# Kernel tuning notes

Measured on AMD Instinct MI355X. Metric: run time of the kernel, lower is better.

The kernel has to match this reference:

```python
import jax, jax.numpy as jnp
import numpy as np

B, F, H, C, K, NHID = 4096, 512, 1024, 100, 32, 3  # NHID = num_layers - 1 hidden->hidden layers


def setup_inputs() -> dict:
    key = jax.random.key(0)
    ks = jax.random.split(key, 5)
    s_in = 1.0 / np.sqrt(F)
    s_h = 1.0 / np.sqrt(H)
    return {
        "x": jax.random.normal(ks[0], (B, F), dtype=jnp.float32),
        "W_in": jax.random.normal(ks[1], (K, F, H), dtype=jnp.float32) * s_in,
        "b_in": jnp.zeros((K, H), dtype=jnp.float32),
        "W_hid": jax.random.normal(ks[2], (NHID, K, H, H), dtype=jnp.float32) * s_h,
        "b_hid": jnp.zeros((NHID, K, H), dtype=jnp.float32),
        "W_out": jax.random.normal(ks[3], (K, H, C), dtype=jnp.float32) * s_h,
        "b_out": jnp.zeros((K, C), dtype=jnp.float32),
    }


def reference(x, W_in, b_in, W_hid, b_hid, W_out, b_out):
    # Batched ensemble: all k MLPs as stacked GEMMs. Dropout off (inference).
    h = jax.nn.relu(jnp.einsum("bf,kfh->kbh", x, W_in) + b_in[:, None, :])  # [K,B,H]
    for i in range(W_hid.shape[0]):  # small fixed layer loop
        h = jax.nn.relu(jnp.einsum("kbh,khj->kbj", h, W_hid[i]) + b_hid[i][:, None, :])
    logits = jnp.einsum("kbh,khc->kbc", h, W_out) + b_out[:, None, :]  # [K,B,C]
    return jnp.mean(logits, axis=0)  # [B,C]
```

## Files before the change

kernel.cpp:

```cpp
#include <hip/hip_runtime.h>
#include <stdint.h>

#define BB   4096
#define FF   512
#define HH   1024
#define CC   100
#define KE   32
#define NHIDL 3
#define CPAD 128

typedef __attribute__((ext_vector_type(8))) short short8;
typedef __attribute__((ext_vector_type(4))) float float4_t;

__device__ __forceinline__ unsigned short f2h(float f) {
  _Float16 h = (_Float16)f;
  union { _Float16 h; unsigned short u; } cv;
  cv.h = h;
  return cv.u;
}

__device__ __forceinline__ void gll16(const void* g, void* l) {
  __builtin_amdgcn_global_load_lds((const __attribute__((address_space(1))) void*)g,
                                   (__attribute__((address_space(3))) void*)l,
                                   16, 0, 0);
}

__global__ void cvt_f16(const float* __restrict__ in, unsigned short* __restrict__ out, int n4) {
  int i = blockIdx.x * 256 + threadIdx.x;
  if (i < n4) {
    float4 v = ((const float4*)in)[i];
    ushort4 o;
    o.x = f2h(v.x); o.y = f2h(v.y); o.z = f2h(v.z); o.w = f2h(v.w);
    ((ushort4*)out)[i] = o;
  }
}

__global__ void transpose_cvt(const float* __restrict__ in, unsigned short* __restrict__ out,
                              int R, int C, int Cpad) {
  __shared__ float tile[32][33];
  int b = blockIdx.z;
  const float* ib = in + (size_t)b * R * C;
  unsigned short* ob = out + (size_t)b * Cpad * R;
  int c0 = blockIdx.x * 32, r0 = blockIdx.y * 32;
  int tx = threadIdx.x & 31, ty = threadIdx.x >> 5;
#pragma unroll
  for (int j = 0; j < 4; ++j) {
    int r = r0 + ty + j * 8, c = c0 + tx;
    tile[ty + j * 8][tx] = (c < C) ? ib[(size_t)r * C + c] : 0.0f;
  }
  __syncthreads();
#pragma unroll
  for (int j = 0; j < 4; ++j) {
    int orow = c0 + ty + j * 8, ocol = r0 + tx;
    if (orow < Cpad) ob[(size_t)orow * R + ocol] = f2h(tile[tx][ty + j * 8]);
  }
}

__global__ void reduce_mean(const float* __restrict__ L, float* __restrict__ out,
                            int n, long long sk) {
  int i = blockIdx.x * 256 + threadIdx.x;
  if (i < n) {
    float s = 0.f;
#pragma unroll
    for (int k = 0; k < KE; ++k) s += L[(long long)k * sk + i];
    out[i] = s * (1.0f / (float)KE);
  }
}

template <int RELU, int FINAL, int KD>
__global__ __launch_bounds__(256, 4) void gemm_f16(
    const unsigned short* __restrict__ A, long long sAk,
    const unsigned short* __restrict__ Bt, long long sBk,
    const float* __restrict__ bias, int sBiasK,
    unsigned short* __restrict__ Out, long long sOutK,
    float* __restrict__ OutF, long long sFk) {
  const int t = threadIdx.x;
  const int lane = t & 63;
  const int wave = t >> 6;
  const int wm = wave & 1;
  const int wn = wave >> 1;
  const int kz = blockIdx.z;
  const int m0 = blockIdx.y * 128;
  const int n0 = blockIdx.x * 128;

  const unsigned short* Ab = A + (long long)kz * sAk + (long long)m0 * KD;
  const unsigned short* Bb = Bt + (long long)kz * sBk + (long long)n0 * KD;

  __shared__ __align__(16) unsigned short smA[128 * 64];
  __shared__ __align__(16) unsigned short smB[128 * 64];

  float4_t acc[4][4];
#pragma unroll
  for (int i = 0; i < 4; ++i)
#pragma unroll
    for (int j = 0; j < 4; ++j) acc[i][j] = (float4_t){0.f, 0.f, 0.f, 0.f};

  int goff[4];
  unsigned short* la[4];
  unsigned short* lb[4];
#pragma unroll
  for (int j = 0; j < 4; ++j) {
    int s = j * 256 + t;
    int row = s >> 3;
    int g = (s & 7) ^ (row & 7);
    goff[j] = row * KD + g * 8;
    la[j] = smA + (size_t)((j * 256 + (t & 0xC0)) * 8);
    lb[j] = smB + (size_t)((j * 256 + (t & 0xC0)) * 8);
  }

  const int r16 = lane & 15;
  const int q = lane >> 4;
  int offA[4][2], offB[4][2];
#pragma unroll
  for (int i = 0; i < 4; ++i) {
#pragma unroll
    for (int kh = 0; kh < 2; ++kh) {
      int ra = wm * 64 + i * 16 + r16;
      offA[i][kh] = ra * 64 + ((((kh * 4 + q)) ^ (ra & 7)) << 3);
      int rb = wn * 64 + i * 16 + r16;
      offB[i][kh] = rb * 64 + ((((kh * 4 + q)) ^ (rb & 7)) << 3);
    }
  }

#pragma unroll
  for (int kt = 0; kt < KD; kt += 64) {
#pragma unroll
    for (int j = 0; j < 4; ++j) gll16(Ab + goff[j] + kt, la[j]);
#pragma unroll
    for (int j = 0; j < 4; ++j) gll16(Bb + goff[j] + kt, lb[j]);
    __syncthreads();

#pragma unroll
    for (int kh = 0; kh < 2; ++kh) {
      short8 af[4], bf[4];
#pragma unroll
      for (int i = 0; i < 4; ++i) af[i] = *(const short8*)(smA + offA[i][kh]);
#pragma unroll
      for (int i = 0; i < 4; ++i) bf[i] = *(const short8*)(smB + offB[i][kh]);
#pragma unroll
      for (int mi = 0; mi < 4; ++mi)
#pragma unroll
        for (int ni = 0; ni < 4; ++ni)
          acc[mi][ni] = __builtin_amdgcn_mfma_f32_16x16x32_f16(af[mi], bf[ni], acc[mi][ni], 0, 0, 0);
    }
    __syncthreads();
  }

  const int rbase = q * 4;
  if (FINAL) {
#pragma unroll
    for (int ni = 0; ni < 4; ++ni) {
      int n = wn * 64 + ni * 16 + r16;
      if (n < CC) {
        float bv = bias[kz * sBiasK + n];
#pragma unroll
        for (int mi = 0; mi < 4; ++mi) {
#pragma unroll
          for (int r = 0; r < 4; ++r) {
            int m = m0 + wm * 64 + mi * 16 + rbase + r;
            OutF[(long long)kz * sFk + (long long)m * CC + n] = acc[mi][ni][r] + bv;
          }
        }
      }
    }
  } else {
#pragma unroll
    for (int ni = 0; ni < 4; ++ni) {
      int n = n0 + wn * 64 + ni * 16 + r16;
      float bv = bias[kz * sBiasK + n];
#pragma unroll
      for (int mi = 0; mi < 4; ++mi) {
        int m = m0 + wm * 64 + mi * 16 + rbase;
        unsigned short* op = Out + (long long)kz * sOutK + (long long)m * HH + n;
#pragma unroll
        for (int r = 0; r < 4; ++r) {
          float v = acc[mi][ni][r] + bv;
          if (RELU) v = fmaxf(v, 0.f);
          op[(long long)r * HH] = f2h(v);
        }
      }
    }
  }
}

template <int RELU, int KD>
__global__ __launch_bounds__(512, 2) void gemm256(
    const unsigned short* __restrict__ A, long long sAk,
    const unsigned short* __restrict__ Bt, long long sBk,
    const float* __restrict__ bias, int sBiasK,
    unsigned short* __restrict__ Out, long long sOutK) {
  static_assert(KD % 128 == 0, "need even K-tile count");
  const int t = threadIdx.x;
  const int lane = t & 63;
  const int wave = t >> 6;
  const int wm = wave >> 2;
  const int wn = wave & 3;
  const int r16 = lane & 15;
  const int q = lane >> 4;

  const int gx = gridDim.x, gy = gridDim.y;
  const int gxy = gx * gy;
  const int nwg = gxy * gridDim.z;
  int flat = blockIdx.x + gx * (blockIdx.y + gy * blockIdx.z);
  int id2 = (flat & 7) * (nwg >> 3) + (flat >> 3);
  const int kz = id2 / gxy;
  int rem = id2 - kz * gxy;
  const int ty = rem / gx;
  const int tx = rem - ty * gx;
  const int m0 = ty * 256;
  const int n0 = tx * 256;

  const unsigned short* Ab = A + (long long)kz * sAk + (long long)m0 * KD;
  const unsigned short* Bb = Bt + (long long)kz * sBk + (long long)n0 * KD;

  __shared__ __align__(16) unsigned short sm[2 * 32768];

  const int gq = (t >> 3) * KD + ((((t & 7) ^ ((t >> 3) & 7))) << 3);
  const int wbase = wave * 512;

  const int x7 = r16 & 7;
  const int xk0 = (q ^ x7) << 3;
  const int xk1 = ((4 + q) ^ x7) << 3;
  const int baseA = (wm * 128 + r16) * 64;
  const int baseB = (wn * 64 + r16) * 64;

  float4_t acc[8][4];
#pragma unroll
  for (int i = 0; i < 8; ++i)
#pragma unroll
    for (int j = 0; j < 4; ++j) acc[i][j] = (float4_t){0.f, 0.f, 0.f, 0.f};

  short8 af[4][2];
  short8 bf[4][2];

#define STGA(BUF, QI, TT) gll16(Ab + (QI) * 64 * KD + (TT) * 64 + gq, \
                                sm + (BUF) * 32768 + (QI) * 4096 + wbase)
#define STGB(BUF, QI, TT) gll16(Bb + (QI) * 64 * KD + (TT) * 64 + gq, \
                                sm + (BUF) * 32768 + 16384 + (QI) * 4096 + wbase)
#define DSA(BUF, MH) do { \
    const unsigned short* pA_ = sm + (BUF) * 32768 + baseA + (MH) * 4096; \
    _Pragma("unroll") for (int i_ = 0; i_ < 4; ++i_) { \
      af[i_][0] = *(const short8*)(pA_ + i_ * 1024 + xk0); \
      af[i_][1] = *(const short8*)(pA_ + i_ * 1024 + xk1); \
    } } while (0)
#define DSB(BUF, NH) do { \
    const unsigned short* pB_ = sm + (BUF) * 32768 + 16384 + baseB + (NH) * 2048; \
    _Pragma("unroll") for (int i_ = 0; i_ < 2; ++i_) { \
      bf[(NH) * 2 + i_][0] = *(const short8*)(pB_ + i_ * 1024 + xk0); \
      bf[(NH) * 2 + i_][1] = *(const short8*)(pB_ + i_ * 1024 + xk1); \
    } } while (0)
#define MM(MH, NH) do { \
    __builtin_amdgcn_s_setprio(1); \
    _Pragma("unroll") for (int kh_ = 0; kh_ < 2; ++kh_) { \
      _Pragma("unroll") for (int mi_ = 0; mi_ < 4; ++mi_) { \
        _Pragma("unroll") for (int ni_ = 0; ni_ < 2; ++ni_) { \
          acc[(MH) * 4 + mi_][(NH) * 2 + ni_] = __builtin_amdgcn_mfma_f32_16x16x32_f16( \
              af[mi_][kh_], bf[(NH) * 2 + ni_][kh_], acc[(MH) * 4 + mi_][(NH) * 2 + ni_], 0, 0, 0); \
        } } } \
    __builtin_amdgcn_s_setprio(0); } while (0)
#define BAR() asm volatile("s_barrier" ::: "memory")
#define VMCNT(n) asm volatile("s_waitcnt vmcnt(" #n ")" ::: "memory")

  STGA(0, 0, 0); STGA(0, 1, 0); STGA(0, 2, 0); STGA(0, 3, 0);
  STGB(0, 0, 0); STGB(0, 1, 0); STGB(0, 2, 0); STGB(0, 3, 0);
  STGA(1, 0, 1); STGA(1, 2, 1);
  STGB(1, 0, 1); STGB(1, 1, 1); STGB(1, 2, 1); STGB(1, 3, 1);
  VMCNT(6);
  BAR();

  const int nT = KD / 64;
  const int nI = nT / 2;
#pragma unroll 1
  for (int j = 0; j < nI - 1; ++j) {
    const int O1 = 2 * j + 1, E2 = 2 * j + 2, O2 = 2 * j + 3;
    DSA(0, 0); DSB(0, 0); STGA(1, 1, O1); STGA(1, 3, O1); MM(0, 0);           BAR();
    DSB(0, 1);            STGA(0, 0, E2); STGA(0, 2, E2); MM(0, 1);           BAR();
    DSA(0, 1);            STGB(0, 0, E2); STGB(0, 1, E2); MM(1, 1);           BAR();
                          STGB(0, 2, E2); STGB(0, 3, E2); MM(1, 0); VMCNT(6); BAR();
    DSA(1, 0); DSB(1, 0); STGA(0, 1, E2); STGA(0, 3, E2); MM(0, 0);           BAR();
    DSB(1, 1);            STGA(1, 0, O2); STGA(1, 2, O2); MM(0, 1);           BAR();
    DSA(1, 1);            STGB(1, 0, O2); STGB(1, 1, O2); MM(1, 1);           BAR();
                          STGB(1, 2, O2); STGB(1, 3, O2); MM(1, 0); VMCNT(6); BAR();
  }
  {
    const int O1 = nT - 1;
    DSA(0, 0); DSB(0, 0); STGA(1, 1, O1); STGA(1, 3, O1); MM(0, 0);           BAR();
    DSB(0, 1);                                            MM(0, 1);           BAR();
    DSA(0, 1);                                            MM(1, 1);           BAR();
                                                          MM(1, 0); VMCNT(0); BAR();
    DSA(1, 0); DSB(1, 0);                                 MM(0, 0);           BAR();
    DSB(1, 1);                                            MM(0, 1);           BAR();
    DSA(1, 1);                                            MM(1, 1);
                                                          MM(1, 0);
  }

  const int rbase = q * 4;
#pragma unroll
  for (int ni = 0; ni < 4; ++ni) {
    const int n = n0 + wn * 64 + ni * 16 + r16;
    const float bv = bias[kz * sBiasK + n];
#pragma unroll
    for (int mi = 0; mi < 8; ++mi) {
      const int m = m0 + wm * 128 + mi * 16 + rbase;
      unsigned short* op = Out + (long long)kz * sOutK + (long long)m * HH + n;
#pragma unroll
      for (int rr = 0; rr < 4; ++rr) {
        float v = acc[mi][ni][rr] + bv;
        if (RELU) v = fmaxf(v, 0.f);
        op[(long long)rr * HH] = f2h(v);
      }
    }
  }
#undef STGA
#undef STGB
#undef DSA
#undef DSB
#undef MM
#undef BAR
#undef VMCNT
}

extern "C" void kernel_launch(void* const* d_in, const int* in_sizes, int n_in,
                              void* d_out, int out_size, void* d_ws, size_t ws_size,
                              hipStream_t stream) {
  (void)in_sizes; (void)n_in; (void)out_size;
  const float* x     = (const float*)d_in[0];
  const float* W_in  = (const float*)d_in[1];
  const float* b_in  = (const float*)d_in[2];
  const float* W_hid = (const float*)d_in[3];
  const float* b_hid = (const float*)d_in[4];
  const float* W_out = (const float*)d_in[5];
  const float* b_out = (const float*)d_in[6];
  float* out = (float*)d_out;

  char* ws = (char*)d_ws;
  size_t off = 0;
  auto alloc = [&](size_t bytes) -> void* {
    void* p = ws + off;
    off += (bytes + 255) & ~(size_t)255;
    return p;
  };
  unsigned short* xb    = (unsigned short*)alloc((size_t)BB * FF * 2);
  unsigned short* WinT  = (unsigned short*)alloc((size_t)KE * HH * FF * 2);
  unsigned short* WhidT = (unsigned short*)alloc((size_t)NHIDL * KE * HH * HH * 2);
  unsigned short* WoutT = (unsigned short*)alloc((size_t)KE * CPAD * HH * 2);
  size_t fixed = off;

  int Bc = BB;
  while (Bc > 128 && fixed + 2 * (size_t)KE * Bc * HH * 2 > ws_size) Bc >>= 1;
  unsigned short* h0 = (unsigned short*)alloc((size_t)KE * Bc * HH * 2);
  unsigned short* h1 = (unsigned short*)alloc((size_t)KE * Bc * HH * 2);

  cvt_f16<<<(BB * FF / 4 + 255) / 256, 256, 0, stream>>>(x, xb, BB * FF / 4);
  transpose_cvt<<<dim3(HH / 32, FF / 32, KE), 256, 0, stream>>>(W_in, WinT, FF, HH, HH);
  transpose_cvt<<<dim3(HH / 32, HH / 32, NHIDL * KE), 256, 0, stream>>>(W_hid, WhidT, HH, HH, HH);
  transpose_cvt<<<dim3(CPAD / 32, HH / 32, KE), 256, 0, stream>>>(W_out, WoutT, HH, CC, CPAD);

  const bool big = (Bc % 256) == 0;

  for (int c0 = 0; c0 < BB; c0 += Bc) {
    if (big) {
      gemm256<1, FF><<<dim3(HH / 256, Bc / 256, KE), 512, 0, stream>>>(
          xb + (size_t)c0 * FF, 0LL, WinT, (long long)HH * FF, b_in, HH,
          h0, (long long)Bc * HH);
    } else {
      gemm_f16<1, 0, FF><<<dim3(HH / 128, Bc / 128, KE), 256, 0, stream>>>(
          xb + (size_t)c0 * FF, 0LL, WinT, (long long)HH * FF, b_in, HH,
          h0, (long long)Bc * HH, nullptr, 0LL);
    }
    unsigned short* hin = h0;
    unsigned short* hout = h1;
    for (int l = 0; l < NHIDL; ++l) {
      if (big) {
        gemm256<1, HH><<<dim3(HH / 256, Bc / 256, KE), 512, 0, stream>>>(
            hin, (long long)Bc * HH, WhidT + (size_t)l * KE * HH * HH, (long long)HH * HH,
            b_hid + (size_t)l * KE * HH, HH, hout, (long long)Bc * HH);
      } else {
        gemm_f16<1, 0, HH><<<dim3(HH / 128, Bc / 128, KE), 256, 0, stream>>>(
            hin, (long long)Bc * HH, WhidT + (size_t)l * KE * HH * HH, (long long)HH * HH,
            b_hid + (size_t)l * KE * HH, HH, hout, (long long)Bc * HH, nullptr, 0LL);
      }
      unsigned short* tmp = hin; hin = hout; hout = tmp;
    }
    float* Lbuf = (float*)hout;
    gemm_f16<0, 1, HH><<<dim3(1, Bc / 128, KE), 256, 0, stream>>>(
        hin, (long long)Bc * HH, WoutT, (long long)CPAD * HH, b_out, CC,
        nullptr, 0LL, Lbuf, (long long)Bc * CC);
    reduce_mean<<<(Bc * CC + 255) / 256, 256, 0, stream>>>(
        Lbuf, out + (size_t)c0 * CC, Bc * CC, (long long)Bc * CC);
  }
}
```

Before: 1.704 ms.

## Restructure GEMM main loop into two phases per tile with fewer barriers

Reorganizes the software-pipelined GEMM loop so each K-tile is processed in two phases instead of four. Each phase issues more LDS fragment reads and global-to-LDS prefetches, then two MFMA quadrants. The prefetch of part of the odd B tile is moved from the prologue into the first phase. This halves the number of s_barrier calls per tile to cut synchronisation stalls. In exchange, more B fragments stay live in registers at once and the vmcnt accounting around LDS buffer reuse becomes more delicate.

```diff
diff --git a/kernel.cpp b/kernel.cpp
--- a/kernel.cpp
+++ b/kernel.cpp
@@ -264,8 +264,8 @@
   STGA(0, 0, 0); STGA(0, 1, 0); STGA(0, 2, 0); STGA(0, 3, 0);
   STGB(0, 0, 0); STGB(0, 1, 0); STGB(0, 2, 0); STGB(0, 3, 0);
   STGA(1, 0, 1); STGA(1, 2, 1);
-  STGB(1, 0, 1); STGB(1, 1, 1); STGB(1, 2, 1); STGB(1, 3, 1);
-  VMCNT(6);
+  STGB(1, 0, 1); STGB(1, 1, 1);
+  VMCNT(4);
   BAR();
 
   const int nT = KD / 64;
@@ -273,25 +273,40 @@
 #pragma unroll 1
   for (int j = 0; j < nI - 1; ++j) {
     const int O1 = 2 * j + 1, E2 = 2 * j + 2, O2 = 2 * j + 3;
-    DSA(0, 0); DSB(0, 0); STGA(1, 1, O1); STGA(1, 3, O1); MM(0, 0);           BAR();
-    DSB(0, 1);            STGA(0, 0, E2); STGA(0, 2, E2); MM(0, 1);           BAR();
-    DSA(0, 1);            STGB(0, 0, E2); STGB(0, 1, E2); MM(1, 1);           BAR();
-                          STGB(0, 2, E2); STGB(0, 3, E2); MM(1, 0); VMCNT(6); BAR();
-    DSA(1, 0); DSB(1, 0); STGA(0, 1, E2); STGA(0, 3, E2); MM(0, 0);           BAR();
-    DSB(1, 1);            STGA(1, 0, O2); STGA(1, 2, O2); MM(0, 1);           BAR();
-    DSA(1, 1);            STGB(1, 0, O2); STGB(1, 1, O2); MM(1, 1);           BAR();
-                          STGB(1, 2, O2); STGB(1, 3, O2); MM(1, 0); VMCNT(6); BAR();
+    DSB(0, 0); DSB(0, 1); DSA(0, 0);
+    STGA(1, 1, O1); STGA(1, 3, O1); STGB(1, 2, O1); STGB(1, 3, O1);
+    MM(0, 0); MM(0, 1);
+    BAR();
+    DSA(0, 1);
+    STGA(0, 0, E2); STGA(0, 2, E2); STGB(0, 0, E2); STGB(0, 1, E2);
+    MM(1, 1); MM(1, 0);
+    VMCNT(4);
+    BAR();
+    DSB(1, 0); DSB(1, 1); DSA(1, 0);
+    STGA(0, 1, E2); STGA(0, 3, E2); STGB(0, 2, E2); STGB(0, 3, E2);
+    MM(0, 0); MM(0, 1);
+    BAR();
+    DSA(1, 1);
+    STGA(1, 0, O2); STGA(1, 2, O2); STGB(1, 0, O2); STGB(1, 1, O2);
+    MM(1, 1); MM(1, 0);
+    VMCNT(4);
+    BAR();
   }
   {
     const int O1 = nT - 1;
-    DSA(0, 0); DSB(0, 0); STGA(1, 1, O1); STGA(1, 3, O1); MM(0, 0);           BAR();
-    DSB(0, 1);                                            MM(0, 1);           BAR();
-    DSA(0, 1);                                            MM(1, 1);           BAR();
-                                                          MM(1, 0); VMCNT(0); BAR();
-    DSA(1, 0); DSB(1, 0);                                 MM(0, 0);           BAR();
-    DSB(1, 1);                                            MM(0, 1);           BAR();
-    DSA(1, 1);                                            MM(1, 1);
-                                                          MM(1, 0);
+    DSB(0, 0); DSB(0, 1); DSA(0, 0);
+    STGA(1, 1, O1); STGA(1, 3, O1); STGB(1, 2, O1); STGB(1, 3, O1);
+    MM(0, 0); MM(0, 1);
+    BAR();
+    DSA(0, 1);
+    MM(1, 1); MM(1, 0);
+    VMCNT(0);
+    BAR();
+    DSB(1, 0); DSB(1, 1); DSA(1, 0);
+    MM(0, 0); MM(0, 1);
+    BAR();
+    DSA(1, 1);
+    MM(1, 1); MM(1, 0);
   }
 
   const int rbase = q * 4;
```

Result: slower. 1.757 ms (+3.1%).
